# Kernel optimization log

Measured on AMD Instinct MI355X. Metric: run time of the kernel, lower is better.

The kernel has to match this reference:

```python
import jax, jax.numpy as jnp
import numpy as np

EPS = 1e-6
LN_EPS = 1e-6

def _mlstm_parallel_stabilized(q, k, v, igate_preact, fgate_preact):
    # q,k,v: (B,NH,S,DH); igate_preact,fgate_preact: (B,NH,S,1)
    B, NH, S, DH = q.shape
    log_fg = jax.nn.log_sigmoid(fgate_preact[..., 0])            # (B,NH,S)
    cs = jnp.cumsum(log_fg, axis=-1)                             # (B,NH,S)
    # log decay matrix: entry (i,j) = cumsum_i - cumsum_j, lower-triangular (j<=i)
    fg_mat = cs[..., :, None] - cs[..., None, :]                 # (B,NH,S,S)
    mask = jnp.tril(jnp.ones((S, S), dtype=bool))
    log_D = jnp.where(mask, fg_mat + igate_preact[..., 0][..., None, :], -jnp.inf)
    max_log_D = jnp.max(log_D, axis=-1, keepdims=True)           # (B,NH,S,1)
    D = jnp.exp(log_D - max_log_D)                               # (B,NH,S,S)
    k_scaled = k / jnp.sqrt(jnp.float32(DH)).astype(k.dtype)
    qk = jnp.einsum('bhsd,bhtd->bhst', q, k_scaled)              # (B,NH,S,S)
    C = qk * D
    normalizer = jnp.maximum(jnp.abs(jnp.sum(C, axis=-1, keepdims=True)), jnp.exp(-max_log_D))
    C_norm = C / (normalizer + EPS)
    return jnp.einsum('bhst,bhtd->bhsd', C_norm, v)              # (B,NH,S,DH)

def _multihead_layernorm(x, weight):
    # x: (B,NH,S,DH), weight: (NH,DH); normalize over DH per head, no bias
    mu = jnp.mean(x, axis=-1, keepdims=True)
    var = jnp.mean(jnp.square(x - mu), axis=-1, keepdims=True)
    xn = (x - mu) * jax.lax.rsqrt(var + LN_EPS)
    return xn * weight[None, :, None, :]

def setup_inputs() -> dict:
    key = jax.random.key(0)
    ks = jax.random.split(key, 6)
    B, S, E, NH = 2, 2048, 1024, 8
    q = jax.random.normal(ks[0], (B, S, E), dtype=jnp.float32)
    k = jax.random.normal(ks[1], (B, S, E), dtype=jnp.float32)
    v = jax.random.normal(ks[2], (B, S, E), dtype=jnp.float32)
    igate_kernel = jnp.zeros((3 * E, NH), dtype=jnp.float32)
    igate_bias = 0.1 * jax.random.normal(ks[3], (NH,), dtype=jnp.float32)
    fgate_kernel = jnp.zeros((3 * E, NH), dtype=jnp.float32)
    fgate_bias = jnp.linspace(3.0, 6.0, NH, dtype=jnp.float32)
    outnorm_weight = jnp.ones((NH, E // NH), dtype=jnp.float32)
    return {"q": q, "k": k, "v": v,
            "igate_kernel": igate_kernel, "igate_bias": igate_bias,
            "fgate_kernel": fgate_kernel, "fgate_bias": fgate_bias,
            "outnorm_weight": outnorm_weight}

def reference(q, k, v, igate_kernel, igate_bias, fgate_kernel, fgate_bias, outnorm_weight):
    B, S, E = q.shape
    NH = igate_bias.shape[0]
    qkv = jnp.concatenate([q, k, v], axis=-1)                    # (B,S,3E)
    igate_preact = qkv @ igate_kernel + igate_bias               # (B,S,NH)
    fgate_preact = qkv @ fgate_kernel + fgate_bias               # (B,S,NH)
    qh = q.reshape(B, S, NH, -1).transpose(0, 2, 1, 3)           # (B,NH,S,DH)
    kh = k.reshape(B, S, NH, -1).transpose(0, 2, 1, 3)
    vh = v.reshape(B, S, NH, -1).transpose(0, 2, 1, 3)
    ig = igate_preact.transpose(0, 2, 1)[..., None]              # (B,NH,S,1)
    fg = fgate_preact.transpose(0, 2, 1)[..., None]
    h = _mlstm_parallel_stabilized(qh, kh, vh, ig, fg)           # (B,NH,S,DH)
    h_norm = _multihead_layernorm(h, outnorm_weight)
    return h_norm.transpose(0, 2, 1, 3).reshape(B, S, -1)        # (B,S,E)
```

## Files before the change

### kernel.cpp

```cpp
#include <hip/hip_runtime.h>
#include <math.h>

#define S_LEN 2048
#define E_DIM 1024
#define NHEAD 8
#define DHEAD 128

typedef short bf16x8 __attribute__((ext_vector_type(8)));
typedef float f32x4 __attribute__((ext_vector_type(4)));
typedef unsigned int u32x4 __attribute__((ext_vector_type(4)));
typedef unsigned int u32x2 __attribute__((ext_vector_type(2)));

constexpr float RSQ_DH  = 0.08838834764831843f;
constexpr float LNRSQ   = -2.4260151319598084f;
constexpr float EPS_NORM = 1e-6f;
constexpr float LN_EPS_C = 1e-6f;

__device__ inline unsigned bfpair(float lo, float hi) {
  unsigned a = __builtin_bit_cast(unsigned, lo);
  unsigned b = __builtin_bit_cast(unsigned, hi);
  a = (a + 0x7fffu + ((a >> 16) & 1u)) >> 16;
  b = (b + 0x7fffu + ((b >> 16) & 1u)) >> 16;
  return a | (b << 16);
}

__device__ inline void gload_lds16(const void* g, void* lds) {
  __builtin_amdgcn_global_load_lds(
      (const __attribute__((address_space(1))) unsigned int*)g,
      (__attribute__((address_space(3))) unsigned int*)lds, 16, 0, 0);
}
__device__ inline void gload_lds4(const void* g, void* lds) {
  __builtin_amdgcn_global_load_lds(
      (const __attribute__((address_space(1))) unsigned int*)g,
      (__attribute__((address_space(3))) unsigned int*)lds, 4, 0, 0);
}

__global__ __launch_bounds__(256) void gates_fused(
    const float* __restrict__ q, const float* __restrict__ k, const float* __restrict__ v,
    const float* __restrict__ Wi, const float* __restrict__ bi,
    const float* __restrict__ Wf, const float* __restrict__ bf,
    float* __restrict__ ig_pre, float* __restrict__ fg_pre,
    unsigned short* __restrict__ kb) {
  const int t = threadIdx.x;
  const int row0 = blockIdx.x * 8;
  const int b = row0 >> 11;
  const int s0 = row0 & 2047;
  float p[8][16];
#pragma unroll
  for (int rr = 0; rr < 8; ++rr)
#pragma unroll
    for (int c = 0; c < 16; ++c) p[rr][c] = 0.f;

#pragma unroll
  for (int i = 0; i < 3; ++i) {
    const float* base = (i == 0) ? q : (i == 1) ? k : v;
    float xs[8][4];
#pragma unroll
    for (int rr = 0; rr < 8; ++rr) {
      const float4 xv = *(const float4*)(base + (size_t)(row0 + rr) * E_DIM + t * 4);
      xs[rr][0] = xv.x; xs[rr][1] = xv.y; xs[rr][2] = xv.z; xs[rr][3] = xv.w;
    }
#pragma unroll
    for (int j = 0; j < 4; ++j) {
      const int ge = i * E_DIM + t * 4 + j;
      const float4 wiA = *(const float4*)(Wi + (size_t)ge * 8);
      const float4 wiB = *(const float4*)(Wi + (size_t)ge * 8 + 4);
      const float4 wfA = *(const float4*)(Wf + (size_t)ge * 8);
      const float4 wfB = *(const float4*)(Wf + (size_t)ge * 8 + 4);
      const float wv16[16] = {wiA.x, wiA.y, wiA.z, wiA.w, wiB.x, wiB.y, wiB.z, wiB.w,
                              wfA.x, wfA.y, wfA.z, wfA.w, wfB.x, wfB.y, wfB.z, wfB.w};
#pragma unroll
      for (int rr = 0; rr < 8; ++rr) {
        const float x = xs[rr][j];
#pragma unroll
        for (int c = 0; c < 16; ++c) p[rr][c] += x * wv16[c];
      }
    }
    if (i == 1 && kb != nullptr) {
      const int h = (t * 4) >> 7, d = (t * 4) & 127;
#pragma unroll
      for (int rr = 0; rr < 8; ++rr) {
        u32x2 pk;
        pk.x = bfpair(xs[rr][0], xs[rr][1]);
        pk.y = bfpair(xs[rr][2], xs[rr][3]);
        *(u32x2*)(kb + (((size_t)b * NHEAD + h) * S_LEN + (s0 + rr)) * DHEAD + d) = pk;
      }
    }
  }

#pragma unroll
  for (int rr = 0; rr < 8; ++rr)
#pragma unroll
    for (int c = 0; c < 16; ++c) {
      float val = p[rr][c];
      val += __shfl_xor(val, 1);
      val += __shfl_xor(val, 2);
      val += __shfl_xor(val, 4);
      val += __shfl_xor(val, 8);
      val += __shfl_xor(val, 16);
      val += __shfl_xor(val, 32);
      p[rr][c] = val;
    }
  __shared__ float sred[4][8][16];
  const int wid = t >> 6, lane = t & 63;
  if (lane == 0) {
#pragma unroll
    for (int rr = 0; rr < 8; ++rr)
#pragma unroll
      for (int c = 0; c < 16; ++c) sred[wid][rr][c] = p[rr][c];
  }
  __syncthreads();
  if (t < 128) {
    const int rr = t >> 4, c = t & 15;
    float sum = sred[0][rr][c] + sred[1][rr][c] + sred[2][rr][c] + sred[3][rr][c];
    const int h = c & 7;
    const int row = row0 + rr;
    const int bb = row / S_LEN, s = row % S_LEN;
    if (c < 8) ig_pre[((size_t)bb * NHEAD + h) * S_LEN + s] = sum + bi[h];
    else       fg_pre[((size_t)bb * NHEAD + h) * S_LEN + s] = sum + bf[h];
  }
}

__global__ __launch_bounds__(256) void vtrans(const float* __restrict__ v,
                                              unsigned short* __restrict__ vtb) {
  __shared__ unsigned int tile[128][36];
  const int bid = blockIdx.x;
  const int bh = bid >> 5, st = bid & 31;
  const int b = bh >> 3, h = bh & 7;
  const int s0 = st * 64;
  const int t = threadIdx.x;
#pragma unroll
  for (int i = 0; i < 4; ++i) {
    const int task = t + 256 * i;
    const int sp = task & 31, dq = task >> 5;
    const float* src = v + ((size_t)b * S_LEN + s0 + 2 * sp) * E_DIM + h * DHEAD + dq * 4;
    const float4 r0 = *(const float4*)(src);
    const float4 r1 = *(const float4*)(src + E_DIM);
    tile[dq * 4 + 0][sp] = bfpair(r0.x, r1.x);
    tile[dq * 4 + 1][sp] = bfpair(r0.y, r1.y);
    tile[dq * 4 + 2][sp] = bfpair(r0.z, r1.z);
    tile[dq * 4 + 3][sp] = bfpair(r0.w, r1.w);
  }
  __syncthreads();
#pragma unroll
  for (int i = 0; i < 2; ++i) {
    const int task = t + 256 * i;
    const int d = task >> 2, c4 = task & 3;
    u32x4 w0, w1;
    w0.x = tile[d][c4 * 8 + 0]; w0.y = tile[d][c4 * 8 + 1];
    w0.z = tile[d][c4 * 8 + 2]; w0.w = tile[d][c4 * 8 + 3];
    w1.x = tile[d][c4 * 8 + 4]; w1.y = tile[d][c4 * 8 + 5];
    w1.z = tile[d][c4 * 8 + 6]; w1.w = tile[d][c4 * 8 + 7];
    unsigned short* dst = vtb + ((size_t)bh * DHEAD + d) * S_LEN + s0 + c4 * 16;
    *(u32x4*)(dst)     = w0;
    *(u32x4*)(dst + 8) = w1;
  }
}

__global__ __launch_bounds__(256) void scan_kernel(
    const float* __restrict__ ig_pre, const float* __restrict__ fg_pre,
    float* __restrict__ cs_out, float* __restrict__ g_out, float* __restrict__ gmax_out,
    float g_add) {
  const int bhh = blockIdx.x;
  const int t = threadIdx.x;
  const size_t base = (size_t)bhh * S_LEN;
  float vals[8];
  float run = 0.f;
#pragma unroll
  for (int i = 0; i < 8; ++i) {
    const float x = fg_pre[base + t * 8 + i];
    const float lf = fminf(x, 0.f) - log1pf(__expf(-fabsf(x)));
    run += lf;
    vals[i] = run;
  }
  __shared__ float sums[256];
  sums[t] = run;
  __syncthreads();
  for (int off = 1; off < 256; off <<= 1) {
    const float other = (t >= off) ? sums[t - off] : 0.f;
    __syncthreads();
    sums[t] += other;
    __syncthreads();
  }
  const float prefix = (t > 0) ? sums[t - 1] : 0.f;
  float g_loc[8], gm_loc[8];
  float lmax = -3.4e38f;
#pragma unroll
  for (int i = 0; i < 8; ++i) {
    const float csv = vals[i] + prefix;
    vals[i] = csv;
    const float gg = ig_pre[base + t * 8 + i] - csv;
    g_loc[i] = gg;
    lmax = fmaxf(lmax, gg);
    gm_loc[i] = lmax;
  }
  __shared__ float maxs[256];
  maxs[t] = lmax;
  __syncthreads();
  for (int off = 1; off < 256; off <<= 1) {
    const float other = (t >= off) ? maxs[t - off] : -3.4e38f;
    __syncthreads();
    maxs[t] = fmaxf(maxs[t], other);
    __syncthreads();
  }
  const float pmax = (t > 0) ? maxs[t - 1] : -3.4e38f;
#pragma unroll
  for (int i = 0; i < 8; ++i) {
    cs_out[base + t * 8 + i]   = vals[i];
    g_out[base + t * 8 + i]    = g_loc[i] + g_add;
    gmax_out[base + t * 8 + i] = fmaxf(gm_loc[i], pmax);
  }
}

__global__ __launch_bounds__(128) void mlstm_mfma3(
    const unsigned short* __restrict__ kb, const unsigned short* __restrict__ vtb,
    const float* __restrict__ q,
    const float* __restrict__ cs, const float* __restrict__ garr, const float* __restrict__ gmax,
    const float* __restrict__ wgt, float* __restrict__ out) {
  __shared__ __align__(16) unsigned char kbuf[2][16384];
  __shared__ __align__(16) unsigned char vbuf[2][16384];
  __shared__ float g_sh[2][64];

  const int bid = blockIdx.x;
  const int bh = 2 * (bid & 7) + ((bid >> 3) & 1);
  const int qb = 63 - (bid >> 4);
  const int b = bh >> 3, h = bh & 7;
  const int t = threadIdx.x;
  const int w = t >> 6;
  const int l = t & 63;
  const int r = l & 15;
  const int qq = l >> 4;
  const size_t bhS = (size_t)bh * S_LEN;

  const int gr = qb * 32 + 2 * r + w;
  const float gm_lane = gmax[bhS + gr];

  bf16x8 qfrag[4];
  {
    const float* qrow = q + ((size_t)b * S_LEN + gr) * E_DIM + h * DHEAD;
#pragma unroll
    for (int c = 0; c < 4; ++c) {
      const float4 f0 = *(const float4*)(qrow + 32 * c + 8 * qq);
      const float4 f1 = *(const float4*)(qrow + 32 * c + 8 * qq + 4);
      u32x4 u;
      u.x = bfpair(f0.x, f0.y); u.y = bfpair(f0.z, f0.w);
      u.z = bfpair(f1.x, f1.y); u.w = bfpair(f1.z, f1.w);
      qfrag[c] = __builtin_bit_cast(bf16x8, u);
    }
  }

  f32x4 o[8];
#pragma unroll
  for (int n = 0; n < 8; ++n) o[n] = (f32x4){0.f, 0.f, 0.f, 0.f};
  float den_p = 0.f;

  const unsigned short* kt = kb + bhS * DHEAD;
  const unsigned short* vt = vtb + (size_t)bh * DHEAD * S_LEN;

  const int ntiles = (qb >> 1) + 1;

  auto stage = [&](int jt_, int bufi) {
    const int j0 = jt_ * 64;
#pragma unroll
    for (int a = 0; a < 8; ++a) {
      const int m = w * 512 + a * 64 + l;
      const int u = m ^ ((m >> 4) & 7);
      const int j = u >> 4, seg = u & 15;
      gload_lds16(kt + ((size_t)(j0 + j)) * DHEAD + seg * 8,
                  &kbuf[bufi][(w * 512 + a * 64) * 16]);
    }
#pragma unroll
    for (int a = 0; a < 8; ++a) {
      const int m = w * 512 + a * 64 + l;
      const int u = m ^ ((m >> 3) & 7);
      const int d = u >> 3, qv = u & 7;
      gload_lds16(vt + (size_t)d * S_LEN + j0 + qv * 8,
                  &vbuf[bufi][(w * 512 + a * 64) * 16]);
    }
    gload_lds4(garr + bhS + j0 + l, &g_sh[bufi][0]);
  };

  stage(0, 0);

  for (int jt = 0; jt < ntiles; ++jt) {
    const int cur = jt & 1;
    if (jt + 1 < ntiles) {
      stage(jt + 1, cur ^ 1);
      asm volatile("s_waitcnt vmcnt(17)" ::: "memory");
    } else {
      asm volatile("s_waitcnt vmcnt(0)" ::: "memory");
    }
    __builtin_amdgcn_sched_barrier(0);
    __syncthreads();
    __builtin_amdgcn_s_setprio(1);
    const int j0 = jt * 64;

    f32x4 st[4];
#pragma unroll
    for (int g = 0; g < 4; ++g) st[g] = (f32x4){0.f, 0.f, 0.f, 0.f};
#pragma unroll
    for (int c = 0; c < 4; ++c) {
#pragma unroll
      for (int g = 0; g < 4; ++g) {
        const int u = ((16 * g + r) * 16 + 4 * c + qq) ^ (r & 7);
        bf16x8 ka = *(const bf16x8*)&kbuf[cur][u * 16];
        st[g] = __builtin_amdgcn_mfma_f32_16x16x32_bf16(ka, qfrag[c], st[g], 0, 0, 0);
      }
    }

    const bool diag = (jt == ntiles - 1);
    unsigned P[4][2];
#pragma unroll
    for (int g = 0; g < 4; ++g) {
      float wv[4];
#pragma unroll
      for (int m = 0; m < 4; ++m) {
        const int jl = 16 * g + 4 * qq + m;
        float ww = st[g][m] * __expf(g_sh[cur][jl] - gm_lane);
        if (diag && (j0 + jl > gr)) ww = 0.f;
        wv[m] = ww;
        den_p += ww;
      }
      P[g][0] = bfpair(wv[0], wv[1]);
      P[g][1] = bfpair(wv[2], wv[3]);
    }

    unsigned A0[4], A1[4];
#pragma unroll
    for (int m = 0; m < 4; ++m) {
      const int srcl = r + 16 * (2 * (qq & 1) + (m >> 1));
      const unsigned x0 = (unsigned)__shfl((int)P[0][m & 1], srcl);
      const unsigned x1 = (unsigned)__shfl((int)P[1][m & 1], srcl);
      const unsigned x2 = (unsigned)__shfl((int)P[2][m & 1], srcl);
      const unsigned x3 = (unsigned)__shfl((int)P[3][m & 1], srcl);
      A0[m] = (qq < 2) ? x0 : x1;
      A1[m] = (qq < 2) ? x2 : x3;
    }
    u32x4 ua0, ua1;
    ua0.x = A0[0]; ua0.y = A0[1]; ua0.z = A0[2]; ua0.w = A0[3];
    ua1.x = A1[0]; ua1.y = A1[1]; ua1.z = A1[2]; ua1.w = A1[3];
    const bf16x8 pa0 = __builtin_bit_cast(bf16x8, ua0);
    const bf16x8 pa1 = __builtin_bit_cast(bf16x8, ua1);

#pragma unroll
    for (int n = 0; n < 8; ++n) {
      const int d = 16 * n + r;
      const int u0 = (d * 8 + qq)     ^ (d & 7);
      const int u1 = (d * 8 + 4 + qq) ^ (d & 7);
      bf16x8 vb0 = *(const bf16x8*)&vbuf[cur][u0 * 16];
      bf16x8 vb1 = *(const bf16x8*)&vbuf[cur][u1 * 16];
      o[n] = __builtin_amdgcn_mfma_f32_16x16x32_bf16(pa0, vb0, o[n], 0, 0, 0);
      o[n] = __builtin_amdgcn_mfma_f32_16x16x32_bf16(pa1, vb1, o[n], 0, 0, 0);
    }
    __builtin_amdgcn_s_setprio(0);
    __syncthreads();
  }

  float den_f = den_p;
  den_f += __shfl_xor(den_f, 16);
  den_f += __shfl_xor(den_f, 32);

  const float* wrow = wgt + h * DHEAD;
  float wv_n[8];
#pragma unroll
  for (int n = 0; n < 8; ++n) wv_n[n] = wrow[16 * n + r];

#pragma unroll
  for (int m = 0; m < 4; ++m) {
    const int iloc = 4 * qq + m;
    const float den_o = __shfl(den_f, iloc);
    const int grow = qb * 32 + 2 * iloc + w;
    const float csg = cs[bhS + grow];
    const float gmg = gmax[bhS + grow];
    const float norm = fmaxf(fabsf(den_o), __expf(-(csg + gmg))) + EPS_NORM;
    const float inv = 1.f / norm;
    float hv[8];
    float s1 = 0.f, s2 = 0.f;
#pragma unroll
    for (int n = 0; n < 8; ++n) {
      hv[n] = o[n][m] * inv;
      s1 += hv[n]; s2 += hv[n] * hv[n];
    }
    s1 += __shfl_xor(s1, 1); s1 += __shfl_xor(s1, 2);
    s1 += __shfl_xor(s1, 4); s1 += __shfl_xor(s1, 8);
    s2 += __shfl_xor(s2, 1); s2 += __shfl_xor(s2, 2);
    s2 += __shfl_xor(s2, 4); s2 += __shfl_xor(s2, 8);
    const float mu  = s1 * (1.f / 128.f);
    const float var = s2 * (1.f / 128.f) - mu * mu;
    const float rstd = rsqrtf(var + LN_EPS_C);
    float* orow = out + ((size_t)b * S_LEN + grow) * E_DIM + h * DHEAD;
#pragma unroll
    for (int n = 0; n < 8; ++n)
      orow[16 * n + r] = (hv[n] - mu) * rstd * wv_n[n];
  }
}

__global__ __launch_bounds__(256) void mlstm_mfma(
    const float* __restrict__ q, const float* __restrict__ k, const float* __restrict__ v,
    const float* __restrict__ cs, const float* __restrict__ garr, const float* __restrict__ gmax,
    const float* __restrict__ wgt, float* __restrict__ out) {
  __shared__ unsigned short k_lds[32][136];
  __shared__ unsigned int   vt_u32[128][20];
  __shared__ unsigned int   xch[4][16][20];
  __shared__ float          g_sh[32];

  const int bid = blockIdx.x;
  int qt;
  if (bid < 256) qt = 31 - (bid >> 4);
  else           qt = (bid - 256) >> 4;
  const int bh = bid & 15;
  const int b = bh >> 3, h = bh & 7;
  const int t = threadIdx.x;
  const int w = t >> 6;
  const int l = t & 63;
  const int r = l & 15;
  const int qq = l >> 4;
  const size_t bhS = (size_t)bh * S_LEN;

  const int gr = qt * 64 + 4 * r + w;
  const float gm_lane = gmax[bhS + gr];

  bf16x8 qfrag[4];
  {
    const float* qrow = q + ((size_t)b * S_LEN + gr) * E_DIM + h * DHEAD;
#pragma unroll
    for (int c = 0; c < 4; ++c) {
      const float4 f0 = *(const float4*)(qrow + 32 * c + 8 * qq);
      const float4 f1 = *(const float4*)(qrow + 32 * c + 8 * qq + 4);
      u32x4 u;
      u.x = bfpair(f0.x, f0.y); u.y = bfpair(f0.z, f0.w);
      u.z = bfpair(f1.x, f1.y); u.w = bfpair(f1.z, f1.w);
      qfrag[c] = __builtin_bit_cast(bf16x8, u);
    }
  }

  f32x4 o[8];
#pragma unroll
  for (int n = 0; n < 8; ++n) o[n] = (f32x4){0.f, 0.f, 0.f, 0.f};
  float den_p = 0.f;

  const int kj = t >> 3, ks = t & 7;
  const int vjp = t & 15, vds = t >> 4;

  const int ntiles = 2 * qt + 2;
  for (int jt = 0; jt < ntiles; ++jt) {
    const int j0 = jt * 32;
    {
      const float* src = k + ((size_t)b * S_LEN + j0 + kj) * E_DIM + h * DHEAD + ks * 16;
      float4 f0 = *(const float4*)(src);
      float4 f1 = *(const float4*)(src + 4);
      float4 f2 = *(const float4*)(src + 8);
      float4 f3 = *(const float4*)(src + 12);
      u32x4 ua, ub;
      ua.x = bfpair(f0.x, f0.y); ua.y = bfpair(f0.z, f0.w);
      ua.z = bfpair(f1.x, f1.y); ua.w = bfpair(f1.z, f1.w);
      ub.x = bfpair(f2.x, f2.y); ub.y = bfpair(f2.z, f2.w);
      ub.z = bfpair(f3.x, f3.y); ub.w = bfpair(f3.z, f3.w);
      *(u32x4*)&k_lds[kj][ks * 16]     = ua;
      *(u32x4*)&k_lds[kj][ks * 16 + 8] = ub;
    }
    {
      const float* s0 = v + ((size_t)b * S_LEN + j0 + 2 * vjp) * E_DIM + h * DHEAD + vds * 8;
      const float* s1 = s0 + E_DIM;
      float4 a0 = *(const float4*)(s0);
      float4 a1 = *(const float4*)(s0 + 4);
      float4 b0 = *(const float4*)(s1);
      float4 b1 = *(const float4*)(s1 + 4);
      vt_u32[vds * 8 + 0][vjp] = bfpair(a0.x, b0.x);
      vt_u32[vds * 8 + 1][vjp] = bfpair(a0.y, b0.y);
      vt_u32[vds * 8 + 2][vjp] = bfpair(a0.z, b0.z);
      vt_u32[vds * 8 + 3][vjp] = bfpair(a0.w, b0.w);
      vt_u32[vds * 8 + 4][vjp] = bfpair(a1.x, b1.x);
      vt_u32[vds * 8 + 5][vjp] = bfpair(a1.y, b1.y);
      vt_u32[vds * 8 + 6][vjp] = bfpair(a1.z, b1.z);
      vt_u32[vds * 8 + 7][vjp] = bfpair(a1.w, b1.w);
    }
    if (t < 32) g_sh[t] = garr[bhS + j0 + t];
    __syncthreads();

    f32x4 st0 = {0, 0, 0, 0}, st1 = {0, 0, 0, 0};
#pragma unroll
    for (int c = 0; c < 4; ++c) {
      bf16x8 ka0 = *(const bf16x8*)&k_lds[r][32 * c + 8 * qq];
      bf16x8 ka1 = *(const bf16x8*)&k_lds[16 + r][32 * c + 8 * qq];
      st0 = __builtin_amdgcn_mfma_f32_16x16x32_bf16(ka0, qfrag[c], st0, 0, 0, 0);
      st1 = __builtin_amdgcn_mfma_f32_16x16x32_bf16(ka1, qfrag[c], st1, 0, 0, 0);
    }

    const bool diag = (jt >= 2 * qt);
    float wv0[4], wv1[4];
#pragma unroll
    for (int reg = 0; reg < 4; ++reg) {
      const int jl0 = 4 * qq + reg, jl1 = 16 + 4 * qq + reg;
      const float e0 = __expf(g_sh[jl0] - gm_lane);
      const float e1 = __expf(g_sh[jl1] - gm_lane);
      float w0 = st0[reg] * RSQ_DH * e0;
      float w1 = st1[reg] * RSQ_DH * e1;
      if (diag) {
        if (j0 + jl0 > gr) w0 = 0.f;
        if (j0 + jl1 > gr) w1 = 0.f;
      }
      wv0[reg] = w0; wv1[reg] = w1;
      den_p += w0 + w1;
    }

    u32x2 p0, p1;
    p0.x = bfpair(wv0[0], wv0[1]); p0.y = bfpair(wv0[2], wv0[3]);
    p1.x = bfpair(wv1[0], wv1[1]); p1.y = bfpair(wv1[2], wv1[3]);
    *(u32x2*)&xch[w][r][2 * qq]     = p0;
    *(u32x2*)&xch[w][r][8 + 2 * qq] = p1;
    __builtin_amdgcn_wave_barrier();
    bf16x8 pa = *(const bf16x8*)&xch[w][r][4 * qq];
    __builtin_amdgcn_wave_barrier();

#pragma unroll
    for (int n = 0; n < 8; ++n) {
      bf16x8 vb = *(const bf16x8*)&vt_u32[16 * n + r][4 * qq];
      o[n] = __builtin_amdgcn_mfma_f32_16x16x32_bf16(pa, vb, o[n], 0, 0, 0);
    }
    __syncthreads();
  }

  float den_f = den_p;
  den_f += __shfl_xor(den_f, 16);
  den_f += __shfl_xor(den_f, 32);

  const float* wrow = wgt + h * DHEAD;
  float wv_n[8];
#pragma unroll
  for (int n = 0; n < 8; ++n) wv_n[n] = wrow[16 * n + r];

#pragma unroll
  for (int reg = 0; reg < 4; ++reg) {
    const int iloc = 4 * qq + reg;
    const float den_o = __shfl(den_f, iloc);
    const int grow = qt * 64 + 4 * iloc + w;
    const float csg = cs[bhS + grow];
    const float gmg = gmax[bhS + grow];
    const float norm = fmaxf(fabsf(den_o), __expf(-(csg + gmg))) + EPS_NORM;
    const float inv = 1.f / norm;
    float hv[8];
    float s1 = 0.f, s2 = 0.f;
#pragma unroll
    for (int n = 0; n < 8; ++n) {
      hv[n] = o[n][reg] * inv;
      s1 += hv[n]; s2 += hv[n] * hv[n];
    }
    s1 += __shfl_xor(s1, 1); s1 += __shfl_xor(s1, 2);
    s1 += __shfl_xor(s1, 4); s1 += __shfl_xor(s1, 8);
    s2 += __shfl_xor(s2, 1); s2 += __shfl_xor(s2, 2);
    s2 += __shfl_xor(s2, 4); s2 += __shfl_xor(s2, 8);
    const float mu  = s1 * (1.f / 128.f);
    const float var = s2 * (1.f / 128.f) - mu * mu;
    const float rstd = rsqrtf(var + LN_EPS_C);
    float* orow = out + ((size_t)b * S_LEN + grow) * E_DIM + h * DHEAD;
#pragma unroll
    for (int n = 0; n < 8; ++n)
      orow[16 * n + r] = (hv[n] - mu) * rstd * wv_n[n];
  }
}

extern "C" void kernel_launch(void* const* d_in, const int* in_sizes, int n_in,
                              void* d_out, int out_size, void* d_ws, size_t ws_size,
                              hipStream_t stream) {
  (void)in_sizes; (void)n_in; (void)out_size;
  const float* q   = (const float*)d_in[0];
  const float* k   = (const float*)d_in[1];
  const float* v   = (const float*)d_in[2];
  const float* Wi  = (const float*)d_in[3];
  const float* bi  = (const float*)d_in[4];
  const float* Wf  = (const float*)d_in[5];
  const float* bf  = (const float*)d_in[6];
  const float* wgt = (const float*)d_in[7];
  float* out = (float*)d_out;
  float* ws  = (float*)d_ws;
  const int BNS = 2 * NHEAD * S_LEN;
  float* ig_pre = ws;
  float* fg_pre = ws + (size_t)BNS;
  float* cs     = ws + (size_t)2 * BNS;
  float* gv     = ws + (size_t)3 * BNS;
  float* gmaxs  = ws + (size_t)4 * BNS;
  unsigned short* kb  = (unsigned short*)(ws + (size_t)5 * BNS);
  unsigned short* vtb = kb + (size_t)16 * S_LEN * DHEAD;

  const size_t need = (size_t)5 * BNS * 4 + (size_t)2 * 16 * S_LEN * DHEAD * 2;

  if (ws_size >= need) {
    gates_fused<<<512, 256, 0, stream>>>(q, k, v, Wi, bi, Wf, bf, ig_pre, fg_pre, kb);
    vtrans<<<512, 256, 0, stream>>>(v, vtb);
    scan_kernel<<<16, 256, 0, stream>>>(ig_pre, fg_pre, cs, gv, gmaxs, LNRSQ);
    mlstm_mfma3<<<1024, 128, 0, stream>>>(kb, vtb, q, cs, gv, gmaxs, wgt, out);
  } else {
    gates_fused<<<512, 256, 0, stream>>>(q, k, v, Wi, bi, Wf, bf, ig_pre, fg_pre, nullptr);
    scan_kernel<<<16, 256, 0, stream>>>(ig_pre, fg_pre, cs, gv, gmaxs, 0.0f);
    mlstm_mfma<<<512, 256, 0, stream>>>(q, k, v, cs, gv, gmaxs, wgt, out);
  }
}
```

Baseline: 116.9 us.

## Use 64-row query blocks with four waves sharing staged K/V tiles

The main mLSTM kernel now runs 256 threads per block, and each block covers 64 query rows instead of 32. The four waves share each staged K/V tile, which halves the global-to-LDS traffic per query row and reduces block count. The block order is also remapped to balance causal work across the grid. The tile loop is unrolled by two with static buffer indices and a peeled diagonal tile. Bf16 packing uses the hardware v_cvt_pk_bf16_f32 instruction, and MFMA priority is raised only around the matrix phases. Possible costs are fewer blocks (512) for occupancy and rounding that may differ slightly from the software bf16 pack.

```diff
diff --git a/kernel.cpp b/kernel.cpp
--- a/kernel.cpp
+++ b/kernel.cpp
@@ -22,6 +22,12 @@
   a = (a + 0x7fffu + ((a >> 16) & 1u)) >> 16;
   b = (b + 0x7fffu + ((b >> 16) & 1u)) >> 16;
   return a | (b << 16);
+}
+
+__device__ inline unsigned cvtpk(float lo, float hi) {
+  unsigned r;
+  asm("v_cvt_pk_bf16_f32 %0, %1, %2" : "=v"(r) : "v"(lo), "v"(hi));
+  return r;
 }
 
 __device__ inline void gload_lds16(const void* g, void* lds) {
@@ -212,7 +218,7 @@
   }
 }
 
-__global__ __launch_bounds__(128) void mlstm_mfma3(
+__global__ __launch_bounds__(256) void mlstm_mfma4(
     const unsigned short* __restrict__ kb, const unsigned short* __restrict__ vtb,
     const float* __restrict__ q,
     const float* __restrict__ cs, const float* __restrict__ garr, const float* __restrict__ gmax,
@@ -222,8 +228,11 @@
   __shared__ float g_sh[2][64];
 
   const int bid = blockIdx.x;
-  const int bh = 2 * (bid & 7) + ((bid >> 3) & 1);
-  const int qb = 63 - (bid >> 4);
+  int qb;
+  if (bid < 256) qb = 31 - (bid >> 4);
+  else           qb = (bid - 256) >> 4;
+  const int g16 = bid & 15;
+  const int bh = 2 * (g16 & 7) + (g16 >> 3);
   const int b = bh >> 3, h = bh & 7;
   const int t = threadIdx.x;
   const int w = t >> 6;
@@ -232,7 +241,7 @@
   const int qq = l >> 4;
   const size_t bhS = (size_t)bh * S_LEN;
 
-  const int gr = qb * 32 + 2 * r + w;
+  const int gr = qb * 64 + 4 * r + w;
   const float gm_lane = gmax[bhS + gr];
 
   bf16x8 qfrag[4];
@@ -257,44 +266,32 @@
   const unsigned short* kt = kb + bhS * DHEAD;
   const unsigned short* vt = vtb + (size_t)bh * DHEAD * S_LEN;
 
-  const int ntiles = (qb >> 1) + 1;
+  const int ntiles = qb + 1;
 
   auto stage = [&](int jt_, int bufi) {
     const int j0 = jt_ * 64;
 #pragma unroll
-    for (int a = 0; a < 8; ++a) {
-      const int m = w * 512 + a * 64 + l;
+    for (int a = 0; a < 4; ++a) {
+      const int m = w * 256 + a * 64 + l;
       const int u = m ^ ((m >> 4) & 7);
       const int j = u >> 4, seg = u & 15;
       gload_lds16(kt + ((size_t)(j0 + j)) * DHEAD + seg * 8,
-                  &kbuf[bufi][(w * 512 + a * 64) * 16]);
-    }
-#pragma unroll
-    for (int a = 0; a < 8; ++a) {
-      const int m = w * 512 + a * 64 + l;
+                  &kbuf[bufi][(w * 256 + a * 64) * 16]);
+    }
+#pragma unroll
+    for (int a = 0; a < 4; ++a) {
+      const int m = w * 256 + a * 64 + l;
       const int u = m ^ ((m >> 3) & 7);
       const int d = u >> 3, qv = u & 7;
       gload_lds16(vt + (size_t)d * S_LEN + j0 + qv * 8,
-                  &vbuf[bufi][(w * 512 + a * 64) * 16]);
+                  &vbuf[bufi][(w * 256 + a * 64) * 16]);
     }
     gload_lds4(garr + bhS + j0 + l, &g_sh[bufi][0]);
   };
 
-  stage(0, 0);
-
-  for (int jt = 0; jt < ntiles; ++jt) {
-    const int cur = jt & 1;
-    if (jt + 1 < ntiles) {
-      stage(jt + 1, cur ^ 1);
-      asm volatile("s_waitcnt vmcnt(17)" ::: "memory");
-    } else {
-      asm volatile("s_waitcnt vmcnt(0)" ::: "memory");
-    }
-    __builtin_amdgcn_sched_barrier(0);
-    __syncthreads();
+  auto body = [&](int jt_, int cur, bool diag) {
+    const int j0 = jt_ * 64;
     __builtin_amdgcn_s_setprio(1);
-    const int j0 = jt * 64;
-
     f32x4 st[4];
 #pragma unroll
     for (int g = 0; g < 4; ++g) st[g] = (f32x4){0.f, 0.f, 0.f, 0.f};
@@ -307,8 +304,8 @@
         st[g] = __builtin_amdgcn_mfma_f32_16x16x32_bf16(ka, qfrag[c], st[g], 0, 0, 0);
       }
     }
-
-    const bool diag = (jt == ntiles - 1);
+    __builtin_amdgcn_s_setprio(0);
+
     unsigned P[4][2];
 #pragma unroll
     for (int g = 0; g < 4; ++g) {
@@ -321,8 +318,8 @@
         wv[m] = ww;
         den_p += ww;
       }
-      P[g][0] = bfpair(wv[0], wv[1]);
-      P[g][1] = bfpair(wv[2], wv[3]);
+      P[g][0] = cvtpk(wv[0], wv[1]);
+      P[g][1] = cvtpk(wv[2], wv[3]);
     }
 
     unsigned A0[4], A1[4];
@@ -342,6 +339,7 @@
     const bf16x8 pa0 = __builtin_bit_cast(bf16x8, ua0);
     const bf16x8 pa1 = __builtin_bit_cast(bf16x8, ua1);
 
+    __builtin_amdgcn_s_setprio(1);
 #pragma unroll
     for (int n = 0; n < 8; ++n) {
       const int d = 16 * n + r;
@@ -353,7 +351,41 @@
       o[n] = __builtin_amdgcn_mfma_f32_16x16x32_bf16(pa1, vb1, o[n], 0, 0, 0);
     }
     __builtin_amdgcn_s_setprio(0);
-    __syncthreads();
+  };
+
+  stage(0, 0);
+  const int M = ntiles - 1;
+  int jt = 0;
+  for (; jt + 2 <= M; jt += 2) {
+    stage(jt + 1, 1);
+    asm volatile("s_waitcnt vmcnt(9)" ::: "memory");
+    __builtin_amdgcn_sched_barrier(0);
+    __syncthreads();
+    body(jt, 0, false);
+    __syncthreads();
+    stage(jt + 2, 0);
+    asm volatile("s_waitcnt vmcnt(9)" ::: "memory");
+    __builtin_amdgcn_sched_barrier(0);
+    __syncthreads();
+    body(jt + 1, 1, false);
+    __syncthreads();
+  }
+  if (jt == M - 1) {
+    stage(M, 1);
+    asm volatile("s_waitcnt vmcnt(9)" ::: "memory");
+    __builtin_amdgcn_sched_barrier(0);
+    __syncthreads();
+    body(jt, 0, false);
+    __syncthreads();
+    asm volatile("s_waitcnt vmcnt(0)" ::: "memory");
+    __builtin_amdgcn_sched_barrier(0);
+    __syncthreads();
+    body(M, 1, true);
+  } else {
+    asm volatile("s_waitcnt vmcnt(0)" ::: "memory");
+    __builtin_amdgcn_sched_barrier(0);
+    __syncthreads();
+    body(M, 0, true);
   }
 
   float den_f = den_p;
@@ -369,7 +401,7 @@
   for (int m = 0; m < 4; ++m) {
     const int iloc = 4 * qq + m;
     const float den_o = __shfl(den_f, iloc);
-    const int grow = qb * 32 + 2 * iloc + w;
+    const int grow = qb * 64 + 4 * iloc + w;
     const float csg = cs[bhS + grow];
     const float gmg = gmax[bhS + grow];
     const float norm = fmaxf(fabsf(den_o), __expf(-(csg + gmg))) + EPS_NORM;
@@ -589,7 +621,7 @@
     gates_fused<<<512, 256, 0, stream>>>(q, k, v, Wi, bi, Wf, bf, ig_pre, fg_pre, kb);
     vtrans<<<512, 256, 0, stream>>>(v, vtb);
     scan_kernel<<<16, 256, 0, stream>>>(ig_pre, fg_pre, cs, gv, gmaxs, LNRSQ);
-    mlstm_mfma3<<<1024, 128, 0, stream>>>(kb, vtb, q, cs, gv, gmaxs, wgt, out);
+    mlstm_mfma4<<<512, 256, 0, stream>>>(kb, vtb, q, cs, gv, gmaxs, wgt, out);
   } else {
     gates_fused<<<512, 256, 0, stream>>>(q, k, v, Wi, bi, Wf, bf, ig_pre, fg_pre, nullptr);
     scan_kernel<<<16, 256, 0, stream>>>(ig_pre, fg_pre, cs, gv, gmaxs, 0.0f);
```

Result: faster. 111.3 us (-4.8%).
